# Kernel tuning notes

Measured on AMD Instinct MI355X. Metric: run time of the kernel, lower is better.

The kernel has to match this reference:

```python
import jax, jax.numpy as jnp
import numpy as np

N = 50000      # nodes
E = 800000     # edges (avg degree 16)
F_IN = 128     # input feature dim
HID = 128      # 2 * out_classes
OUT = 64       # out_classes


def setup_inputs() -> dict:
    key = jax.random.key(0)
    ks = jax.random.split(key, 12)
    x = jax.random.normal(ks[0], (N, F_IN), jnp.float32)
    edge_index = jax.random.randint(ks[1], (2, E), 0, N, jnp.int32)
    def lin(k, fi, fo):
        return jax.random.normal(k, (fi, fo), jnp.float32) / np.float32(np.sqrt(fi))
    return {
        "x": x,
        "edge_index": edge_index,
        "W1": lin(ks[2], F_IN, HID), "b1": jnp.zeros((HID,), jnp.float32),
        "W2": lin(ks[3], HID, HID),  "b2": jnp.zeros((HID,), jnp.float32),
        "W3": lin(ks[4], HID, HID),  "b3": jnp.zeros((HID,), jnp.float32),
        "jk_w": jax.random.normal(ks[5], (3,), jnp.float32),
        "fc_W": lin(ks[6], HID, OUT), "fc_b": jnp.zeros((OUT,), jnp.float32),
    }


def _gcn_conv(h, W, b, row, col, n):
    """PyG GCNConv: linear -> add self-loops -> sym-normalized aggregate -> bias."""
    h = h @ W                                        # [n, d_out]
    loops = jnp.arange(n, dtype=row.dtype)
    r = jnp.concatenate([row, loops])                # sources
    c = jnp.concatenate([col, loops])                # targets
    deg = jax.ops.segment_sum(jnp.ones_like(c, h.dtype), c, num_segments=n)
    dinv = jnp.where(deg > 0, jax.lax.rsqrt(deg), 0.0)
    norm = dinv[r] * dinv[c]                         # [E+n]
    msg = h[r] * norm[:, None]                       # gather + scale
    return jax.ops.segment_sum(msg, c, num_segments=n) + b


def _neighbor_mean(h, row, col, n):
    """sample_neighbors with scale_factor=2: exact mean over out-neighbors,
    own feature when degree == 0 (top-k branch is provably dead code)."""
    s = jax.ops.segment_sum(h[col], row, num_segments=n)
    deg = jax.ops.segment_sum(jnp.ones_like(row, h.dtype), row, num_segments=n)
    mean = s / jnp.maximum(deg, 1.0)[:, None]
    return jnp.where((deg > 0)[:, None], mean, h)


def reference(x, edge_index, W1, b1, W2, b2, W3, b3, jk_w, fc_W, fc_b):
    row, col = edge_index[0], edge_index[1]
    n = x.shape[0]
    # layer 0: GCN -> ReLU -> (dropout: eval identity) -> neighbor sampling
    h0 = jax.nn.relu(_gcn_conv(x, W1, b1, row, col, n))
    h0 = _neighbor_mean(h0, row, col, n)
    # layer 1: GCN -> ReLU; historical-activation update is identity on first call
    h1 = jax.nn.relu(_gcn_conv(h0, W2, b2, row, col, n))
    # layer 2
    h2 = jax.nn.relu(_gcn_conv(h1, W3, b3, row, col, n))
    # dynamic JK aggregation
    w = jax.nn.softmax(jk_w)
    h = w[0] * h0 + w[1] * h1 + w[2] * h2
    return h @ fc_W + fc_b
```

## Files before the change

kernel.cpp:

```cpp
#include <hip/hip_runtime.h>
#include <stdint.h>

typedef unsigned int  uint32;
typedef unsigned short u16;

typedef short bfx8 __attribute__((ext_vector_type(8)));
typedef float f32x4 __attribute__((ext_vector_type(4)));
typedef float f32x2 __attribute__((ext_vector_type(2)));
typedef uint32 u32x4 __attribute__((ext_vector_type(4)));

#define NBP 256
#define CH  2048
#define BS  4608

__device__ __forceinline__ float b2f(u16 u) {
    union { uint32 i; float f; } v; v.i = ((uint32)u) << 16; return v.f;
}
__device__ __forceinline__ u16 f2b(float f) {
    union { float f; uint32 i; } v; v.f = f;
    uint32 u = v.i;
    return (u16)((u + 0x7fffu + ((u >> 16) & 1u)) >> 16);
}
__device__ __forceinline__ float blo(uint32 u) {
    union { uint32 i; float f; } v; v.i = u << 16; return v.f;
}
__device__ __forceinline__ float bhi(uint32 u) {
    union { uint32 i; float f; } v; v.i = u & 0xffff0000u; return v.f;
}
__device__ __forceinline__ uint32 packbf(float a, float b) {
    return (uint32)f2b(a) | ((uint32)f2b(b) << 16);
}
__device__ __forceinline__ void splitf(float x, u16& h, u16& l) {
    h = f2b(x);
    l = f2b(x - b2f(h));
}
__device__ __forceinline__ void acc4(float* s, u32x4 v) {
    s[0] += blo(v.x); s[1] += bhi(v.x);
    s[2] += blo(v.y); s[3] += bhi(v.y);
    s[4] += blo(v.z); s[5] += bhi(v.z);
    s[6] += blo(v.w); s[7] += bhi(v.w);
}

__global__ __launch_bounds__(256) void k_init(
    int* __restrict__ curC, int* __restrict__ curR,
    const float* __restrict__ W1, const float* __restrict__ W2,
    const float* __restrict__ W3, const float* __restrict__ fcW,
    u16* __restrict__ WTh, u16* __restrict__ WTl, int WTN) {
    int t = threadIdx.x;
    if (blockIdx.x == 0) {
        curC[t] = t * BS;
        curR[t] = t * BS;
        return;
    }
    int i = ((int)blockIdx.x - 1) * 256 + t;
    if (i >= WTN) return;
    float w;
    if (i < 3 * 16384) {
        int m = i >> 14, j = i & 16383;
        int fo = j >> 7, fi = j & 127;
        const float* W = (m == 0) ? W1 : (m == 1) ? W2 : W3;
        w = W[fi * 128 + fo];
    } else {
        int j = i - 3 * 16384;
        int fo = j >> 7, fi = j & 127;
        w = fcW[fi * 64 + fo];
    }
    u16 h, l; splitf(w, h, l);
    WTh[i] = h; WTl[i] = l;
}

__global__ __launch_bounds__(256) void k_partC(
    const int* __restrict__ row, const int* __restrict__ col, int E,
    int* __restrict__ curC, int* __restrict__ curR,
    uint32* __restrict__ partC, uint32* __restrict__ partR) {
    __shared__ uint32 stagedC[CH], stagedR[CH];
    __shared__ int hp[NBP], expk[NBP], curp[NBP], runC[NBP], runR[NBP];
    __shared__ int wsum[4];
    int t = threadIdx.x;
    int lane = t & 63, wid = t >> 6;
    int base = blockIdx.x * CH;
    int n = E - base; if (n > CH) n = CH;

    int er[8], ec[8];
#pragma unroll
    for (int j = 0; j < 8; ++j) {
        int i = t + j * 256;
        if (i < n) { er[j] = row[base + i]; ec[j] = col[base + i]; }
        else er[j] = -1;
    }
    hp[t] = 0;
    __syncthreads();
#pragma unroll
    for (int j = 0; j < 8; ++j) {
        if (er[j] >= 0) {
            atomicAdd(&hp[ec[j] >> 8], 1);
            atomicAdd(&hp[er[j] >> 8], 0x10000);
        }
    }
    __syncthreads();
    int v = hp[t];
    int x = v;
#pragma unroll
    for (int d = 1; d < 64; d <<= 1) {
        int u = __shfl_up(x, d);
        if (lane >= d) x += u;
    }
    if (lane == 63) wsum[wid] = x;
    __syncthreads();
    int add = 0;
    for (int i = 0; i < wid; ++i) add += wsum[i];
    int ex = x + add - v;
    expk[t] = ex;
    curp[t] = ex;
    int vC = v & 0xffff, vR = v >> 16;
    runC[t] = vC ? atomicAdd(&curC[t], vC) : 0;
    runR[t] = vR ? atomicAdd(&curR[t], vR) : 0;
    __syncthreads();
#pragma unroll
    for (int j = 0; j < 8; ++j) {
        if (er[j] >= 0) {
            int cb = ec[j] >> 8, rb = er[j] >> 8;
            int pC = atomicAdd(&curp[cb], 1) & 0xffff;
            stagedC[pC] = ((uint32)ec[j] << 16) | (uint32)er[j];
            int pR = atomicAdd(&curp[rb], 0x10000) >> 16;
            stagedR[pR] = ((uint32)er[j] << 16) | (uint32)ec[j];
        }
    }
    __syncthreads();
    for (int i = t; i < n; i += 256) {
        uint32 pv = stagedC[i];
        int b = pv >> 24;
        partC[runC[b] + (i - (expk[b] & 0xffff))] = pv;
    }
    for (int i = t; i < n; i += 256) {
        uint32 pv = stagedR[i];
        int b = pv >> 24;
        partR[runR[b] + (i - (expk[b] >> 16))] = pv;
    }
}

__global__ __launch_bounds__(256) void k_fillD(
    const uint32* __restrict__ partC, const uint32* __restrict__ partR,
    const int* __restrict__ curC, const int* __restrict__ curR,
    int* __restrict__ off_in, int* __restrict__ end_in,
    int* __restrict__ off_out, int* __restrict__ end_out,
    u16* __restrict__ csr_src, u16* __restrict__ csr_dst,
    float* __restrict__ dinv, int NB, int N) {
    int part = ((int)blockIdx.x >= NB) ? 1 : 0;
    int b = (int)blockIdx.x - part * NB;
    const uint32* arr = part ? partR : partC;
    const int* curA   = part ? curR : curC;
    int* offA         = part ? off_out : off_in;
    int* endA         = part ? end_out : end_in;
    u16* csr          = part ? csr_dst : csr_src;
    int t = threadIdx.x;
    int lane = t & 63, wid = t >> 6;
    int base = b * BS, end = curA[b];
    __shared__ int cnt[NBP], cur[NBP];
    __shared__ int wsum[4];
    cnt[t] = 0;
    __syncthreads();
    for (int i = base + t; i < end; i += 256)
        atomicAdd(&cnt[(arr[i] >> 16) & 255], 1);
    __syncthreads();
    int v = cnt[t];
    int x = v;
#pragma unroll
    for (int d = 1; d < 64; d <<= 1) {
        int u = __shfl_up(x, d);
        if (lane >= d) x += u;
    }
    if (lane == 63) wsum[wid] = x;
    __syncthreads();
    int add = 0;
    for (int i = 0; i < wid; ++i) add += wsum[i];
    int ex = x + add - v;
    cur[t] = ex;
    int node = (b << 8) + t;
    if (node < N) {
        offA[node] = base + ex;
        endA[node] = base + ex + v;
        if (part == 0) dinv[node] = rsqrtf((float)(v + 1));
    }
    __syncthreads();
    for (int i = base + t; i < end; i += 256) {
        uint32 pv = arr[i];
        int local = (pv >> 16) & 255;
        int pos = atomicAdd(&cur[local], 1);
        csr[base + pos] = (u16)(pv & 0xffffu);
    }
}

__global__ __launch_bounds__(256) void k_gemm0(
    const float* __restrict__ A, const u16* __restrict__ WTh, const u16* __restrict__ WTl,
    const float* __restrict__ dinv, u16* __restrict__ G, int M) {
    const int lane = threadIdx.x & 63;
    const int q = lane >> 4, l = lane & 15;
    int rbase = blockIdx.x * 128 + (threadIdx.x >> 6) * 32;
    if (rbase >= M) return;
    int r0 = rbase + l;      if (r0 >= M) r0 = M - 1;
    int r1 = rbase + 16 + l; if (r1 >= M) r1 = M - 1;

    f32x4 acc[2][8];
#pragma unroll
    for (int i = 0; i < 2; ++i)
#pragma unroll
        for (int j = 0; j < 8; ++j) acc[i][j] = (f32x4){0.f, 0.f, 0.f, 0.f};

#pragma unroll
    for (int kc = 0; kc < 4; ++kc) {
        int k0 = kc * 32 + q * 8;
        bfx8 ah0, ah1;
        {
            f32x4 a = *(const f32x4*)(A + (size_t)r0 * 128 + k0);
            f32x4 b = *(const f32x4*)(A + (size_t)r0 * 128 + k0 + 4);
            float xx[8] = {a[0], a[1], a[2], a[3], b[0], b[1], b[2], b[3]};
#pragma unroll
            for (int j = 0; j < 8; ++j) ah0[j] = (short)f2b(xx[j]);
        }
        {
            f32x4 a = *(const f32x4*)(A + (size_t)r1 * 128 + k0);
            f32x4 b = *(const f32x4*)(A + (size_t)r1 * 128 + k0 + 4);
            float xx[8] = {a[0], a[1], a[2], a[3], b[0], b[1], b[2], b[3]};
#pragma unroll
            for (int j = 0; j < 8; ++j) ah1[j] = (short)f2b(xx[j]);
        }
#pragma unroll
        for (int ct = 0; ct < 8; ++ct) {
            bfx8 bh = *(const bfx8*)(WTh + (ct * 16 + l) * 128 + k0);
            bfx8 bl = *(const bfx8*)(WTl + (ct * 16 + l) * 128 + k0);
            acc[0][ct] = __builtin_amdgcn_mfma_f32_16x16x32_bf16(ah0, bh, acc[0][ct], 0, 0, 0);
            acc[0][ct] = __builtin_amdgcn_mfma_f32_16x16x32_bf16(ah0, bl, acc[0][ct], 0, 0, 0);
            acc[1][ct] = __builtin_amdgcn_mfma_f32_16x16x32_bf16(ah1, bh, acc[1][ct], 0, 0, 0);
            acc[1][ct] = __builtin_amdgcn_mfma_f32_16x16x32_bf16(ah1, bl, acc[1][ct], 0, 0, 0);
        }
    }
#pragma unroll
    for (int rs = 0; rs < 2; ++rs) {
#pragma unroll
        for (int rr = 0; rr < 4; ++rr) {
            int rw = rbase + rs * 16 + q * 4 + rr;
            if (rw < M) {
                float dv = dinv[rw];
#pragma unroll
                for (int ct = 0; ct < 8; ++ct)
                    G[(size_t)rw * 128 + ct * 16 + l] = f2b(acc[rs][ct][rr] * dv);
            }
        }
    }
}

__global__ __launch_bounds__(256) void k_gemm1p(
    const u16* __restrict__ Ah,
    const u16* __restrict__ WTh, const u16* __restrict__ WTl,
    const float* __restrict__ dinv, u16* __restrict__ G, int M) {
    const int lane = threadIdx.x & 63;
    const int q = lane >> 4, l = lane & 15;
    int rbase = blockIdx.x * 128 + (threadIdx.x >> 6) * 32;
    if (rbase >= M) return;
    int r0 = rbase + l;      if (r0 >= M) r0 = M - 1;
    int r1 = rbase + 16 + l; if (r1 >= M) r1 = M - 1;

    f32x4 acc[2][8];
#pragma unroll
    for (int i = 0; i < 2; ++i)
#pragma unroll
        for (int j = 0; j < 8; ++j) acc[i][j] = (f32x4){0.f, 0.f, 0.f, 0.f};

#pragma unroll
    for (int kc = 0; kc < 4; ++kc) {
        int k0 = kc * 32 + q * 8;
        bfx8 ah0 = *(const bfx8*)(Ah + (size_t)r0 * 128 + k0);
        bfx8 ah1 = *(const bfx8*)(Ah + (size_t)r1 * 128 + k0);
#pragma unroll
        for (int ct = 0; ct < 8; ++ct) {
            bfx8 bh = *(const bfx8*)(WTh + (ct * 16 + l) * 128 + k0);
            bfx8 bl = *(const bfx8*)(WTl + (ct * 16 + l) * 128 + k0);
            acc[0][ct] = __builtin_amdgcn_mfma_f32_16x16x32_bf16(ah0, bh, acc[0][ct], 0, 0, 0);
            acc[0][ct] = __builtin_amdgcn_mfma_f32_16x16x32_bf16(ah0, bl, acc[0][ct], 0, 0, 0);
            acc[1][ct] = __builtin_amdgcn_mfma_f32_16x16x32_bf16(ah1, bh, acc[1][ct], 0, 0, 0);
            acc[1][ct] = __builtin_amdgcn_mfma_f32_16x16x32_bf16(ah1, bl, acc[1][ct], 0, 0, 0);
        }
    }
#pragma unroll
    for (int rs = 0; rs < 2; ++rs) {
#pragma unroll
        for (int rr = 0; rr < 4; ++rr) {
            int rw = rbase + rs * 16 + q * 4 + rr;
            if (rw < M) {
                float dv = dinv[rw];
#pragma unroll
                for (int ct = 0; ct < 8; ++ct)
                    G[(size_t)rw * 128 + ct * 16 + l] = f2b(acc[rs][ct][rr] * dv);
            }
        }
    }
}

__global__ __launch_bounds__(256) void k_agg(
    const u32x4* __restrict__ g4, const u16* __restrict__ csr,
    const int* __restrict__ off, const int* __restrict__ endo,
    const float* __restrict__ dinv,
    const float* __restrict__ bias, u32x4* __restrict__ outH4, int n) {
    int w = (blockIdx.x * 256 + threadIdx.x) >> 6;
    if (w >= n) return;
    int lane = threadIdx.x & 63;
    int gq = lane >> 4, c = lane & 15;
    float s[8];
#pragma unroll
    for (int k = 0; k < 8; ++k) s[k] = 0.f;
    int e = off[w], e1 = endo[w];
    for (; e + 16 <= e1; e += 16) {
        int i0 = csr[e + gq];
        int i1 = csr[e + 4 + gq];
        int i2 = csr[e + 8 + gq];
        int i3 = csr[e + 12 + gq];
        u32x4 v0 = g4[(size_t)i0 * 16 + c];
        u32x4 v1 = g4[(size_t)i1 * 16 + c];
        u32x4 v2 = g4[(size_t)i2 * 16 + c];
        u32x4 v3 = g4[(size_t)i3 * 16 + c];
        acc4(s, v0); acc4(s, v1); acc4(s, v2); acc4(s, v3);
    }
    for (; e < e1; e += 4) {
        int idx = e + gq;
        if (idx < e1) {
            int ii = csr[idx];
            acc4(s, g4[(size_t)ii * 16 + c]);
        }
    }
#pragma unroll
    for (int k = 0; k < 8; ++k) {
        s[k] += __shfl_xor(s[k], 16);
        s[k] += __shfl_xor(s[k], 32);
    }
    if (lane < 16) {
        u32x4 sv = g4[(size_t)w * 16 + lane];
        s[0] += blo(sv.x); s[1] += bhi(sv.x);
        s[2] += blo(sv.y); s[3] += bhi(sv.y);
        s[4] += blo(sv.z); s[5] += bhi(sv.z);
        s[6] += blo(sv.w); s[7] += bhi(sv.w);
        float dc = dinv[w];
        const f32x4* B4 = (const f32x4*)bias;
        f32x4 ba = B4[lane * 2], bb = B4[lane * 2 + 1];
        float o[8];
#pragma unroll
        for (int k = 0; k < 4; ++k) o[k] = fmaxf(fmaf(s[k], dc, ba[k]), 0.f);
#pragma unroll
        for (int k = 0; k < 4; ++k) o[4 + k] = fmaxf(fmaf(s[4 + k], dc, bb[k]), 0.f);
        u32x4 ov;
        ov.x = packbf(o[0], o[1]); ov.y = packbf(o[2], o[3]);
        ov.z = packbf(o[4], o[5]); ov.w = packbf(o[6], o[7]);
        outH4[(size_t)w * 16 + lane] = ov;
    }
}

__global__ __launch_bounds__(256) void k_mean(
    const u32x4* __restrict__ h4, const u16* __restrict__ csr,
    const int* __restrict__ off, const int* __restrict__ endo,
    u32x4* __restrict__ outH4, int n) {
    int w = (blockIdx.x * 256 + threadIdx.x) >> 6;
    if (w >= n) return;
    int lane = threadIdx.x & 63;
    int gq = lane >> 4, c = lane & 15;
    float s[8];
#pragma unroll
    for (int k = 0; k < 8; ++k) s[k] = 0.f;
    int e = off[w], e1 = endo[w];
    int d = e1 - e;
    for (; e + 16 <= e1; e += 16) {
        int i0 = csr[e + gq];
        int i1 = csr[e + 4 + gq];
        int i2 = csr[e + 8 + gq];
        int i3 = csr[e + 12 + gq];
        u32x4 v0 = h4[(size_t)i0 * 16 + c];
        u32x4 v1 = h4[(size_t)i1 * 16 + c];
        u32x4 v2 = h4[(size_t)i2 * 16 + c];
        u32x4 v3 = h4[(size_t)i3 * 16 + c];
        acc4(s, v0); acc4(s, v1); acc4(s, v2); acc4(s, v3);
    }
    for (; e < e1; e += 4) {
        int idx = e + gq;
        if (idx < e1) {
            int ii = csr[idx];
            acc4(s, h4[(size_t)ii * 16 + c]);
        }
    }
#pragma unroll
    for (int k = 0; k < 8; ++k) {
        s[k] += __shfl_xor(s[k], 16);
        s[k] += __shfl_xor(s[k], 32);
    }
    if (lane < 16) {
        u32x4 ov;
        if (d > 0) {
            float inv = 1.f / (float)d;
            ov.x = packbf(s[0] * inv, s[1] * inv);
            ov.y = packbf(s[2] * inv, s[3] * inv);
            ov.z = packbf(s[4] * inv, s[5] * inv);
            ov.w = packbf(s[6] * inv, s[7] * inv);
        } else {
            ov = h4[(size_t)w * 16 + lane];
        }
        outH4[(size_t)w * 16 + lane] = ov;
    }
}

__global__ __launch_bounds__(256) void k_final(
    const u16* __restrict__ h0, const u16* __restrict__ h1,
    const u16* __restrict__ h2, const float* __restrict__ jkw,
    const u16* __restrict__ fcWTh, const u16* __restrict__ fcWTl,
    const float* __restrict__ fcb, float* __restrict__ out, int M) {
    float a0 = jkw[0], a1 = jkw[1], a2 = jkw[2];
    float mx = fmaxf(a0, fmaxf(a1, a2));
    float e0 = expf(a0 - mx), e1 = expf(a1 - mx), e2 = expf(a2 - mx);
    float inv = 1.f / (e0 + e1 + e2);
    float w0 = e0 * inv, w1 = e1 * inv, w2 = e2 * inv;

    const int lane = threadIdx.x & 63;
    const int q = lane >> 4, l = lane & 15;
    int rbase = blockIdx.x * 128 + (threadIdx.x >> 6) * 32;
    if (rbase >= M) return;
    int r0 = rbase + l;      if (r0 >= M) r0 = M - 1;
    int r1 = rbase + 16 + l; if (r1 >= M) r1 = M - 1;

    f32x4 acc[2][4];
#pragma unroll
    for (int i = 0; i < 2; ++i)
#pragma unroll
        for (int j = 0; j < 4; ++j) acc[i][j] = (f32x4){0.f, 0.f, 0.f, 0.f};

    union U8 { bfx8 v; u16 u[8]; };

#pragma unroll
    for (int kc = 0; kc < 4; ++kc) {
        int k0 = kc * 32 + q * 8;
        bfx8 ah[2];
        const int rr2[2] = {r0, r1};
#pragma unroll
        for (int half = 0; half < 2; ++half) {
            size_t o = (size_t)rr2[half] * 128 + k0;
            U8 x0, x1, x2, rh;
            x0.v = *(const bfx8*)(h0 + o);
            x1.v = *(const bfx8*)(h1 + o);
            x2.v = *(const bfx8*)(h2 + o);
#pragma unroll
            for (int j = 0; j < 8; ++j) {
                float c = w0 * b2f(x0.u[j]) + w1 * b2f(x1.u[j]) + w2 * b2f(x2.u[j]);
                rh.u[j] = f2b(c);
            }
            ah[half] = rh.v;
        }
#pragma unroll
        for (int ct = 0; ct < 4; ++ct) {
            bfx8 bh = *(const bfx8*)(fcWTh + (ct * 16 + l) * 128 + k0);
            bfx8 bl = *(const bfx8*)(fcWTl + (ct * 16 + l) * 128 + k0);
#pragma unroll
            for (int half = 0; half < 2; ++half) {
                acc[half][ct] = __builtin_amdgcn_mfma_f32_16x16x32_bf16(ah[half], bh, acc[half][ct], 0, 0, 0);
                acc[half][ct] = __builtin_amdgcn_mfma_f32_16x16x32_bf16(ah[half], bl, acc[half][ct], 0, 0, 0);
            }
        }
    }
#pragma unroll
    for (int rs = 0; rs < 2; ++rs) {
#pragma unroll
        for (int rr = 0; rr < 4; ++rr) {
            int rw = rbase + rs * 16 + q * 4 + rr;
            if (rw < M) {
#pragma unroll
                for (int ct = 0; ct < 4; ++ct) {
                    int cc = ct * 16 + l;
                    out[(size_t)rw * 64 + cc] = acc[rs][ct][rr] + fcb[cc];
                }
            }
        }
    }
}

extern "C" void kernel_launch(void* const* d_in, const int* in_sizes, int n_in,
                              void* d_out, int out_size, void* d_ws, size_t ws_size,
                              hipStream_t stream) {
    const int N = in_sizes[0] / 128;
    const int E = in_sizes[1] / 2;
    const int NB = (N + 255) >> 8;

    const float* x    = (const float*)d_in[0];
    const int* row    = (const int*)d_in[1];
    const int* col    = row + E;
    const float* W1   = (const float*)d_in[2];
    const float* b1   = (const float*)d_in[3];
    const float* W2   = (const float*)d_in[4];
    const float* b2   = (const float*)d_in[5];
    const float* W3   = (const float*)d_in[6];
    const float* b3   = (const float*)d_in[7];
    const float* jkw  = (const float*)d_in[8];
    const float* fcW  = (const float*)d_in[9];
    const float* fcb  = (const float*)d_in[10];
    float* outp       = (float*)d_out;

    char* ws = (char*)d_ws;
    size_t off = 0;
    auto alloc = [&](size_t bytes) -> char* {
        char* p = ws + off;
        off += (bytes + 255) & ~(size_t)255;
        return p;
    };
    int* curC   = (int*)alloc((size_t)NBP * sizeof(int));
    int* curR   = (int*)alloc((size_t)NBP * sizeof(int));
    int* off_in  = (int*)alloc((size_t)N * sizeof(int));
    int* end_in  = (int*)alloc((size_t)N * sizeof(int));
    int* off_out = (int*)alloc((size_t)N * sizeof(int));
    int* end_out = (int*)alloc((size_t)N * sizeof(int));
    uint32* partC = (uint32*)alloc((size_t)NBP * BS * sizeof(uint32));
    uint32* partR = (uint32*)alloc((size_t)NBP * BS * sizeof(uint32));
    u16* csr_src = (u16*)alloc((size_t)NBP * BS * sizeof(u16));
    u16* csr_dst = (u16*)alloc((size_t)NBP * BS * sizeof(u16));
    float* dinv  = (float*)alloc((size_t)N * sizeof(float));
    const int WTN = 3 * 16384 + 8192;
    u16* WTh = (u16*)alloc((size_t)WTN * sizeof(u16));
    u16* WTl = (u16*)alloc((size_t)WTN * sizeof(u16));
    size_t FB = (size_t)N * 128 * sizeof(u16);
    u16* gbuf = (u16*)alloc(FB);
    u16* t0   = (u16*)alloc(FB);
    u16* h0   = (u16*)alloc(FB);
    u16* h1   = (u16*)alloc(FB);
    u16* h2   = (u16*)alloc(FB);

    const int B = 256;
    int Gh = (E + CH - 1) / CH;
    int Gg = (N + 127) / 128;
    int Gwt = (WTN + B - 1) / B;

    k_init<<<1 + Gwt, B, 0, stream>>>(curC, curR, W1, W2, W3, fcW, WTh, WTl, WTN);
    k_partC<<<Gh, B, 0, stream>>>(row, col, E, curC, curR, partC, partR);
    k_fillD<<<2 * NB, B, 0, stream>>>(partC, partR, curC, curR,
                                      off_in, end_in, off_out, end_out,
                                      csr_src, csr_dst, dinv, NB, N);
    k_gemm0<<<Gg, B, 0, stream>>>(x, WTh, WTl, dinv, gbuf, N);

    int aggG = (N + 3) / 4;

    k_agg<<<aggG, B, 0, stream>>>((const u32x4*)gbuf, csr_src, off_in, end_in, dinv,
                                  b1, (u32x4*)t0, N);
    k_mean<<<aggG, B, 0, stream>>>((const u32x4*)t0, csr_dst, off_out, end_out,
                                   (u32x4*)h0, N);
    k_gemm1p<<<Gg, B, 0, stream>>>(h0, WTh + 16384, WTl + 16384, dinv, gbuf, N);
    k_agg<<<aggG, B, 0, stream>>>((const u32x4*)gbuf, csr_src, off_in, end_in, dinv,
                                  b2, (u32x4*)h1, N);
    k_gemm1p<<<Gg, B, 0, stream>>>(h1, WTh + 2 * 16384, WTl + 2 * 16384, dinv, gbuf, N);
    k_agg<<<aggG, B, 0, stream>>>((const u32x4*)gbuf, csr_src, off_in, end_in, dinv,
                                  b3, (u32x4*)h2, N);
    k_final<<<Gg, B, 0, stream>>>(h0, h1, h2, jkw,
                                  WTh + 3 * 16384, WTl + 3 * 16384, fcb, outp, N);
}
```

Baseline: 331.0 us.

## Split feature matrices into four column slabs so aggregation gathers fit cache

```diff
diff --git a/kernel.cpp b/kernel.cpp
--- a/kernel.cpp
+++ b/kernel.cpp
@@ -12,6 +12,7 @@
 #define NBP 256
 #define CH  2048
 #define BS  4608
+
 
 __device__ __forceinline__ float b2f(u16 u) {
     union { uint32 i; float f; } v; v.i = ((uint32)u) << 16; return v.f;
@@ -196,6 +197,7 @@
     const float* __restrict__ dinv, u16* __restrict__ G, int M) {
     const int lane = threadIdx.x & 63;
     const int q = lane >> 4, l = lane & 15;
+    const size_t N32 = (size_t)M * 32;
     int rbase = blockIdx.x * 128 + (threadIdx.x >> 6) * 32;
     if (rbase >= M) return;
     int r0 = rbase + l;      if (r0 >= M) r0 = M - 1;
@@ -243,8 +245,10 @@
             if (rw < M) {
                 float dv = dinv[rw];
 #pragma unroll
-                for (int ct = 0; ct < 8; ++ct)
-                    G[(size_t)rw * 128 + ct * 16 + l] = f2b(acc[rs][ct][rr] * dv);
+                for (int ct = 0; ct < 8; ++ct) {
+                    int p = ct >> 1, j = (ct & 1) * 16 + l;
+                    G[(size_t)p * N32 + (size_t)rw * 32 + j] = f2b(acc[rs][ct][rr] * dv);
+                }
             }
         }
     }
@@ -256,6 +260,7 @@
     const float* __restrict__ dinv, u16* __restrict__ G, int M) {
     const int lane = threadIdx.x & 63;
     const int q = lane >> 4, l = lane & 15;
+    const size_t N32 = (size_t)M * 32;
     int rbase = blockIdx.x * 128 + (threadIdx.x >> 6) * 32;
     if (rbase >= M) return;
     int r0 = rbase + l;      if (r0 >= M) r0 = M - 1;
@@ -270,8 +275,8 @@
 #pragma unroll
     for (int kc = 0; kc < 4; ++kc) {
         int k0 = kc * 32 + q * 8;
-        bfx8 ah0 = *(const bfx8*)(Ah + (size_t)r0 * 128 + k0);
-        bfx8 ah1 = *(const bfx8*)(Ah + (size_t)r1 * 128 + k0);
+        bfx8 ah0 = *(const bfx8*)(Ah + (size_t)kc * N32 + (size_t)r0 * 32 + q * 8);
+        bfx8 ah1 = *(const bfx8*)(Ah + (size_t)kc * N32 + (size_t)r1 * 32 + q * 8);
 #pragma unroll
         for (int ct = 0; ct < 8; ++ct) {
             bfx8 bh = *(const bfx8*)(WTh + (ct * 16 + l) * 128 + k0);
@@ -290,58 +295,53 @@
             if (rw < M) {
                 float dv = dinv[rw];
 #pragma unroll
-                for (int ct = 0; ct < 8; ++ct)
-                    G[(size_t)rw * 128 + ct * 16 + l] = f2b(acc[rs][ct][rr] * dv);
+                for (int ct = 0; ct < 8; ++ct) {
+                    int p = ct >> 1, j = (ct & 1) * 16 + l;
+                    G[(size_t)p * N32 + (size_t)rw * 32 + j] = f2b(acc[rs][ct][rr] * dv);
+                }
             }
         }
     }
 }
 
-__global__ __launch_bounds__(256) void k_agg(
-    const u32x4* __restrict__ g4, const u16* __restrict__ csr,
+__global__ __launch_bounds__(256) void k_aggS(
+    const u32x4* __restrict__ T, const u16* __restrict__ csr,
     const int* __restrict__ off, const int* __restrict__ endo,
-    const float* __restrict__ dinv,
-    const float* __restrict__ bias, u32x4* __restrict__ outH4, int n) {
-    int w = (blockIdx.x * 256 + threadIdx.x) >> 6;
+    const float* __restrict__ dinv, const float* __restrict__ bias,
+    u32x4* __restrict__ outT, int n, int G1) {
+    int blk = (int)blockIdx.x;
+    int p = blk / G1;
+    int nb = blk - p * G1;
+    int w = nb * 4 + (int)(threadIdx.x >> 6);
     if (w >= n) return;
     int lane = threadIdx.x & 63;
-    int gq = lane >> 4, c = lane & 15;
+    int g = lane >> 2, c = lane & 3;
+    const u32x4* Tp = T + (size_t)p * n * 4;
     float s[8];
 #pragma unroll
     for (int k = 0; k < 8; ++k) s[k] = 0.f;
     int e = off[w], e1 = endo[w];
     for (; e + 16 <= e1; e += 16) {
-        int i0 = csr[e + gq];
-        int i1 = csr[e + 4 + gq];
-        int i2 = csr[e + 8 + gq];
-        int i3 = csr[e + 12 + gq];
-        u32x4 v0 = g4[(size_t)i0 * 16 + c];
-        u32x4 v1 = g4[(size_t)i1 * 16 + c];
-        u32x4 v2 = g4[(size_t)i2 * 16 + c];
-        u32x4 v3 = g4[(size_t)i3 * 16 + c];
-        acc4(s, v0); acc4(s, v1); acc4(s, v2); acc4(s, v3);
-    }
-    for (; e < e1; e += 4) {
-        int idx = e + gq;
-        if (idx < e1) {
-            int ii = csr[idx];
-            acc4(s, g4[(size_t)ii * 16 + c]);
-        }
+        int i0 = csr[e + g];
+        acc4(s, Tp[(size_t)i0 * 4 + c]);
+    }
+    if (e < e1) {
+        int idx = e + g;
+        if (idx < e1) acc4(s, Tp[(size_t)csr[idx] * 4 + c]);
     }
 #pragma unroll
     for (int k = 0; k < 8; ++k) {
+        s[k] += __shfl_xor(s[k], 4);
+        s[k] += __shfl_xor(s[k], 8);
         s[k] += __shfl_xor(s[k], 16);
         s[k] += __shfl_xor(s[k], 32);
     }
-    if (lane < 16) {
-        u32x4 sv = g4[(size_t)w * 16 + lane];
-        s[0] += blo(sv.x); s[1] += bhi(sv.x);
-        s[2] += blo(sv.y); s[3] += bhi(sv.y);
-        s[4] += blo(sv.z); s[5] += bhi(sv.z);
-        s[6] += blo(sv.w); s[7] += bhi(sv.w);
+    if (g == 0) {
+        u32x4 sv = Tp[(size_t)w * 4 + c];
+        acc4(s, sv);
         float dc = dinv[w];
-        const f32x4* B4 = (const f32x4*)bias;
-        f32x4 ba = B4[lane * 2], bb = B4[lane * 2 + 1];
+        const f32x4* B4 = (const f32x4*)(bias + p * 32 + c * 8);
+        f32x4 ba = B4[0], bb = B4[1];
         float o[8];
 #pragma unroll
         for (int k = 0; k < 4; ++k) o[k] = fmaxf(fmaf(s[k], dc, ba[k]), 0.f);
@@ -350,47 +350,43 @@
         u32x4 ov;
         ov.x = packbf(o[0], o[1]); ov.y = packbf(o[2], o[3]);
         ov.z = packbf(o[4], o[5]); ov.w = packbf(o[6], o[7]);
-        outH4[(size_t)w * 16 + lane] = ov;
-    }
-}
-
-__global__ __launch_bounds__(256) void k_mean(
-    const u32x4* __restrict__ h4, const u16* __restrict__ csr,
+        outT[(size_t)p * n * 4 + (size_t)w * 4 + c] = ov;
+    }
+}
+
+__global__ __launch_bounds__(256) void k_meanS(
+    const u32x4* __restrict__ T, const u16* __restrict__ csr,
     const int* __restrict__ off, const int* __restrict__ endo,
-    u32x4* __restrict__ outH4, int n) {
-    int w = (blockIdx.x * 256 + threadIdx.x) >> 6;
+    u32x4* __restrict__ outT, int n, int G1) {
+    int blk = (int)blockIdx.x;
+    int p = blk / G1;
+    int nb = blk - p * G1;
+    int w = nb * 4 + (int)(threadIdx.x >> 6);
     if (w >= n) return;
     int lane = threadIdx.x & 63;
-    int gq = lane >> 4, c = lane & 15;
+    int g = lane >> 2, c = lane & 3;
+    const u32x4* Tp = T + (size_t)p * n * 4;
     float s[8];
 #pragma unroll
     for (int k = 0; k < 8; ++k) s[k] = 0.f;
     int e = off[w], e1 = endo[w];
     int d = e1 - e;
     for (; e + 16 <= e1; e += 16) {
-        int i0 = csr[e + gq];
-        int i1 = csr[e + 4 + gq];
-        int i2 = csr[e + 8 + gq];
-        int i3 = csr[e + 12 + gq];
-        u32x4 v0 = h4[(size_t)i0 * 16 + c];
-        u32x4 v1 = h4[(size_t)i1 * 16 + c];
-        u32x4 v2 = h4[(size_t)i2 * 16 + c];
-        u32x4 v3 = h4[(size_t)i3 * 16 + c];
-        acc4(s, v0); acc4(s, v1); acc4(s, v2); acc4(s, v3);
-    }
-    for (; e < e1; e += 4) {
-        int idx = e + gq;
-        if (idx < e1) {
-            int ii = csr[idx];
-            acc4(s, h4[(size_t)ii * 16 + c]);
-        }
+        int i0 = csr[e + g];
+        acc4(s, Tp[(size_t)i0 * 4 + c]);
+    }
+    if (e < e1) {
+        int idx = e + g;
+        if (idx < e1) acc4(s, Tp[(size_t)csr[idx] * 4 + c]);
     }
 #pragma unroll
     for (int k = 0; k < 8; ++k) {
+        s[k] += __shfl_xor(s[k], 4);
+        s[k] += __shfl_xor(s[k], 8);
         s[k] += __shfl_xor(s[k], 16);
         s[k] += __shfl_xor(s[k], 32);
     }
-    if (lane < 16) {
+    if (g == 0) {
         u32x4 ov;
         if (d > 0) {
             float inv = 1.f / (float)d;
@@ -399,9 +395,9 @@
             ov.z = packbf(s[4] * inv, s[5] * inv);
             ov.w = packbf(s[6] * inv, s[7] * inv);
         } else {
-            ov = h4[(size_t)w * 16 + lane];
-        }
-        outH4[(size_t)w * 16 + lane] = ov;
+            ov = Tp[(size_t)w * 4 + c];
+        }
+        outT[(size_t)p * n * 4 + (size_t)w * 4 + c] = ov;
     }
 }
 
@@ -418,6 +414,7 @@
 
     const int lane = threadIdx.x & 63;
     const int q = lane >> 4, l = lane & 15;
+    const size_t N32 = (size_t)M * 32;
     int rbase = blockIdx.x * 128 + (threadIdx.x >> 6) * 32;
     if (rbase >= M) return;
     int r0 = rbase + l;      if (r0 >= M) r0 = M - 1;
@@ -438,7 +435,7 @@
         const int rr2[2] = {r0, r1};
 #pragma unroll
         for (int half = 0; half < 2; ++half) {
-            size_t o = (size_t)rr2[half] * 128 + k0;
+            size_t o = (size_t)kc * N32 + (size_t)rr2[half] * 32 + q * 8;
             U8 x0, x1, x2, rh;
             x0.v = *(const bfx8*)(h0 + o);
             x1.v = *(const bfx8*)(h1 + o);
@@ -538,18 +535,19 @@
                                       csr_src, csr_dst, dinv, NB, N);
     k_gemm0<<<Gg, B, 0, stream>>>(x, WTh, WTl, dinv, gbuf, N);
 
-    int aggG = (N + 3) / 4;
-
-    k_agg<<<aggG, B, 0, stream>>>((const u32x4*)gbuf, csr_src, off_in, end_in, dinv,
-                                  b1, (u32x4*)t0, N);
-    k_mean<<<aggG, B, 0, stream>>>((const u32x4*)t0, csr_dst, off_out, end_out,
-                                   (u32x4*)h0, N);
+    int G1 = (N + 3) / 4;
+    int aggG = 4 * G1;
+
+    k_aggS<<<aggG, B, 0, stream>>>((const u32x4*)gbuf, csr_src, off_in, end_in, dinv,
+                                   b1, (u32x4*)t0, N, G1);
+    k_meanS<<<aggG, B, 0, stream>>>((const u32x4*)t0, csr_dst, off_out, end_out,
+                                    (u32x4*)h0, N, G1);
     k_gemm1p<<<Gg, B, 0, stream>>>(h0, WTh + 16384, WTl + 16384, dinv, gbuf, N);
-    k_agg<<<aggG, B, 0, stream>>>((const u32x4*)gbuf, csr_src, off_in, end_in, dinv,
-                                  b2, (u32x4*)h1, N);
+    k_aggS<<<aggG, B, 0, stream>>>((const u32x4*)gbuf, csr_src, off_in, end_in, dinv,
+                                   b2, (u32x4*)h1, N, G1);
     k_gemm1p<<<Gg, B, 0, stream>>>(h1, WTh + 2 * 16384, WTl + 2 * 16384, dinv, gbuf, N);
-    k_agg<<<aggG, B, 0, stream>>>((const u32x4*)gbuf, csr_src, off_in, end_in, dinv,
-                                  b3, (u32x4*)h2, N);
+    k_aggS<<<aggG, B, 0, stream>>>((const u32x4*)gbuf, csr_src, off_in, end_in, dinv,
+                                   b3, (u32x4*)h2, N, G1);
     k_final<<<Gg, B, 0, stream>>>(h0, h1, h2, jkw,
                                   WTh + 3 * 16384, WTl + 3 * 16384, fcb, outp, N);
 }
```

Result: slower. 491.9 us (+48.6%).
